# Kernel tuning notes

Hardware: AMD Instinct MI355X
Metric: run time of the kernel (lower is better)

## Reference

```python
import jax, jax.numpy as jnp
import numpy as np

EPS = 1e-5
GROUPS = 32


def conv1x1(x, W, b):
    # x: (B,C,T), W: (O,C), b: (O,)
    return jnp.einsum('bct,oc->bot', x, W) + b[None, :, None]


def group_norm(x, gamma, beta):
    B, C, T = x.shape
    xg = x.reshape(B, GROUPS, (C // GROUPS) * T)
    mu = xg.mean(axis=-1, keepdims=True)
    var = xg.var(axis=-1, keepdims=True)
    xn = ((xg - mu) * jax.lax.rsqrt(var + EPS)).reshape(B, C, T)
    return xn * gamma[None, :, None] + beta[None, :, None]


def block(x, W, b, gamma, beta):
    return jax.nn.relu(group_norm(conv1x1(x, W, b), gamma, beta))


def setup_inputs() -> dict:
    key = jax.random.key(0)
    ks = jax.random.split(key, 8)
    B, C, P, T, TF = 4, 512, 512, 2048, 4096
    inp = {
        'feature': jax.random.normal(ks[0], (B, C, T), jnp.float32),
        'frame_level_feature': jax.random.uniform(ks[1], (B, C, TF), jnp.float32),
        # cur_point_conv: conv1x1 C->P + GN(32,P)
        'W1': jax.random.normal(ks[2], (P, C), jnp.float32) / np.sqrt(C),
        'b1': jnp.zeros((P,), jnp.float32),
        'g1': jnp.ones((P,), jnp.float32),
        'be1': jnp.zeros((P,), jnp.float32),
        # lr_conv: conv1x1 C->2P + GN(32,2P)
        'W2': jax.random.normal(ks[3], (2 * P, C), jnp.float32) / np.sqrt(C),
        'b2': jnp.zeros((2 * P,), jnp.float32),
        'g2': jnp.ones((2 * P,), jnp.float32),
        'be2': jnp.zeros((2 * P,), jnp.float32),
        # proposal_conv: conv1x1 4P->C + GN(32,C)
        'W3': jax.random.normal(ks[4], (C, 4 * P), jnp.float32) / np.sqrt(4 * P),
        'b3': jnp.zeros((C,), jnp.float32),
        'g3': jnp.ones((C,), jnp.float32),
        'be3': jnp.zeros((C,), jnp.float32),
    }
    return inp


def reference(feature, frame_level_feature, W1, b1, g1, be1, W2, b2, g2, be2, W3, b3, g3, be3):
    fm_short = block(feature, W1, b1, g1, be1)          # (B,P,T)
    feat = block(feature, W2, b2, g2, be2)              # (B,2P,T)
    t = feature.shape[2]
    # inverse-CDF resampling (uses batch 0 statistics, as original)
    mean_values = frame_level_feature.mean(axis=1)[0]   # (TF,)
    mean_values = mean_values / mean_values.sum()
    cdf = (jnp.cumsum(mean_values) * t).astype(jnp.int32)
    cdf = jnp.minimum(cdf, t - 1)                       # (TF,)
    # exact vectorization of findNearNum loop: first index with minimal |cdf-i|
    targets = jnp.arange(t, dtype=jnp.int32)
    idx = jnp.argmin(jnp.abs(cdf[None, :] - targets[:, None]), axis=1)  # (t,)
    sampled = frame_level_feature[:, :, idx]            # (B,C,t)
    mixed = jnp.concatenate([sampled, feat, fm_short], axis=1)  # (B,4P,t)
    mixed = block(mixed, W3, b3, g3, be3)               # (B,C,t)
    return (mixed, feat)
```

## Files before the change

kernel.cpp:

```cpp
#include <hip/hip_runtime.h>

typedef unsigned short u16;
typedef unsigned int   u32;
typedef __attribute__((ext_vector_type(8))) short short8;
typedef __attribute__((ext_vector_type(4))) float f32x4;

__device__ __forceinline__ float bf2f(u16 v) {
  return __uint_as_float(((u32)v) << 16);
}
__device__ __forceinline__ u16 f2bf(float f) {
  u32 u = __float_as_uint(f);
  u32 r = (u + 0x7FFFu + ((u >> 16) & 1u)) >> 16;
  return (u16)r;
}
__device__ __forceinline__ float relu(float x) { return x < 0.f ? 0.f : x; }

__device__ __forceinline__ void gld16(const void* g, void* l) {
  __builtin_amdgcn_global_load_lds((const __attribute__((address_space(1))) u32*)g,
                                   (__attribute__((address_space(3))) u32*)l, 16, 0, 0);
}

__global__ void colmean_part_kernel(const float* __restrict__ frame,
                                    double* __restrict__ partD) {
  int tf = blockIdx.x * 256 + threadIdx.x;
  int ch = blockIdx.y;
  const float* f0 = frame + tf + (size_t)ch * 64 * 4096;
  double s = 0.0;
  for (int c = 0; c < 64; ++c) s += (double)f0[(size_t)c * 4096];
  partD[ch * 4096 + tf] = s;
}

__global__ void scanD_kernel(const double* __restrict__ partD, int* __restrict__ cdf) {
  __shared__ double part[256];
  __shared__ double base[256];
  __shared__ double Ss;
  int tid = threadIdx.x;
  double loc[16];
  double s = 0.0;
#pragma unroll
  for (int i = 0; i < 16; ++i) {
    int tf = tid * 16 + i;
    double m = 0.0;
#pragma unroll
    for (int ch = 0; ch < 8; ++ch) m += partD[ch * 4096 + tf];
    loc[i] = m / 512.0;
    s += loc[i];
  }
  part[tid] = s;
  __syncthreads();
  if (tid == 0) {
    double t = 0.0;
    for (int i = 0; i < 256; ++i) t += part[i];
    Ss = t;
  }
  __syncthreads();
  double S = Ss;
  s = 0.0;
#pragma unroll
  for (int i = 0; i < 16; ++i) { loc[i] = loc[i] / S; s += loc[i]; }
  part[tid] = s;
  __syncthreads();
  if (tid == 0) {
    double c = 0.0;
    for (int i = 0; i < 256; ++i) { base[i] = c; c += part[i]; }
  }
  __syncthreads();
  double c = base[tid];
#pragma unroll
  for (int i = 0; i < 16; ++i) {
    c += loc[i];
    int iv = (int)(c * 2048.0);
    cdf[tid * 16 + i] = iv < 2047 ? iv : 2047;
  }
}

__global__ void argmin_kernel(const int* __restrict__ cdf, int* __restrict__ idx) {
  __shared__ int sd[256], sj[256];
  int target = blockIdx.x;
  int tid = threadIdx.x;
  int best = 0x7fffffff, bj = 0x7fffffff;
  for (int j = tid; j < 4096; j += 256) {
    int d = cdf[j] - target; d = d < 0 ? -d : d;
    if (d < best) { best = d; bj = j; }
  }
  sd[tid] = best; sj[tid] = bj;
  __syncthreads();
  for (int s = 128; s > 0; s >>= 1) {
    if (tid < s) {
      if (sd[tid+s] < sd[tid] || (sd[tid+s] == sd[tid] && sj[tid+s] < sj[tid])) {
        sd[tid] = sd[tid+s]; sj[tid] = sj[tid+s];
      }
    }
    __syncthreads();
  }
  if (tid == 0) idx[target] = sj[0];
}

__global__ void gatherT_kernel(const float* __restrict__ frame, const int* __restrict__ idx,
                               u16* __restrict__ X3T) {
  __shared__ u16 tile[64][65];
  __shared__ int sidx[64];
  int cb = blockIdx.x * 64, t0 = blockIdx.y * 64, b = blockIdx.z;
  int tid = threadIdx.x;
  if (tid < 64) {
    int it = idx[t0 + tid];
    sidx[tid] = it < 0 ? 0 : (it > 4095 ? 4095 : it);
  }
  __syncthreads();
  const float* fb = frame + (size_t)b * 512 * 4096;
  for (int i = tid; i < 4096; i += 256) {
    int r = i >> 6, tt = i & 63;
    tile[tt][r] = f2bf(fb[(size_t)(cb + r) * 4096 + sidx[tt]]);
  }
  __syncthreads();
  u16* xb = X3T + (size_t)b * 2048 * 2048;
  for (int i = tid; i < 4096; i += 256) {
    int r = i >> 6, cc = i & 63;
    xb[(size_t)(t0 + r) * 2048 + cb + cc] = tile[r][cc];
  }
}

__global__ void transposeCT_kernel(const float* __restrict__ X, u16* __restrict__ XT) {
  __shared__ u16 tile[64][65];
  int cb = blockIdx.x * 64, t0 = blockIdx.y * 64, b = blockIdx.z;
  int tid = threadIdx.x;
  const float* xb = X + (size_t)b * 512 * 2048;
  for (int i = tid; i < 4096; i += 256) {
    int r = i >> 6, tt = i & 63;
    tile[tt][r] = f2bf(xb[(size_t)(cb + r) * 2048 + t0 + tt]);
  }
  __syncthreads();
  u16* xtb = XT + (size_t)b * 2048 * 512;
  for (int i = tid; i < 4096; i += 256) {
    int r = i >> 6, cc = i & 63;
    xtb[(size_t)(t0 + r) * 512 + cb + cc] = tile[r][cc];
  }
}

__global__ void convW12_kernel(const float* __restrict__ W1, const float* __restrict__ W2,
                               u16* __restrict__ dst) {
  int i = blockIdx.x * 256 + threadIdx.x;
  dst[i] = f2bf(i < 262144 ? W1[i] : W2[i - 262144]);
}
__global__ void convW_kernel(const float* __restrict__ src, u16* __restrict__ dst, int n) {
  int i = blockIdx.x * 256 + threadIdx.x;
  if (i < n) dst[i] = f2bf(src[i]);
}

__global__ __launch_bounds__(128) void gemm12_kernel(
    const u16* __restrict__ A, const u16* __restrict__ Bt,
    const float* __restrict__ b1, const float* __restrict__ b2,
    float* __restrict__ Y, float* __restrict__ raw1, float* __restrict__ raw2)
{
  const int K = 512;
  __shared__ short As[2][2048];
  __shared__ short Bs[2][4096];
  const int tid = threadIdx.x;
  const int lane = tid & 63;
  const int w = tid >> 6;
  const int nt = blockIdx.x, mt = blockIdx.y, bb = blockIdx.z;
  const u16* Ab = A + (size_t)mt * 64 * K;
  const u16* Bb = Bt + ((size_t)bb * 2048 + (size_t)nt * 128) * K;
  const int lm = lane & 15, lq = lane >> 4;
  f32x4 acc[4][4] = {};

  auto stage = [&](int buf, int kt) {
#pragma unroll
    for (int p = 0; p < 2; ++p) {
      int chunk = tid + 128 * p;
      int row = chunk >> 2;
      int ko = ((chunk & 3) ^ ((row >> 1) & 3)) << 3;
      gld16(Ab + (size_t)row * K + kt + ko, (char*)As[buf] + chunk * 16);
    }
#pragma unroll
    for (int p = 0; p < 4; ++p) {
      int chunk = tid + 128 * p;
      int row = chunk >> 2;
      int ko = ((chunk & 3) ^ ((row >> 1) & 3)) << 3;
      gld16(Bb + (size_t)row * K + kt + ko, (char*)Bs[buf] + chunk * 16);
    }
  };

  stage(0, 0);
  for (int s = 0; s < 16; ++s) {
    int cur = s & 1;
    __syncthreads();
    if (s + 1 < 16) stage(cur ^ 1, (s + 1) << 5);
    short8 af[4], bfv[4];
#pragma unroll
    for (int i = 0; i < 4; ++i) {
      int r = i * 16 + lm;
      af[i] = *(const short8*)(As[cur] + r * 32 + ((lq ^ ((r >> 1) & 3)) << 3));
    }
#pragma unroll
    for (int j = 0; j < 4; ++j) {
      int r = w * 64 + j * 16 + lm;
      bfv[j] = *(const short8*)(Bs[cur] + r * 32 + ((lq ^ ((r >> 1) & 3)) << 3));
    }
#pragma unroll
    for (int i = 0; i < 4; ++i)
#pragma unroll
      for (int j = 0; j < 4; ++j)
        acc[i][j] = __builtin_amdgcn_mfma_f32_16x16x32_bf16(af[i], bfv[j], acc[i][j], 0, 0, 0);
  }

  float s1[4] = {0.f, 0.f, 0.f, 0.f};
  float s2[4] = {0.f, 0.f, 0.f, 0.f};
#pragma unroll
  for (int i = 0; i < 4; ++i) {
    int mbase = mt * 64 + i * 16 + lq * 4;
#pragma unroll
    for (int e = 0; e < 4; ++e) {
      int m = mbase + e;
      float bv = m < 512 ? b1[m] : b2[m - 512];
      float* yp = Y + ((size_t)bb * 1536 + m) * 2048 + nt * 128 + w * 64 + lm;
#pragma unroll
      for (int j = 0; j < 4; ++j) {
        float v = acc[i][j][e] + bv;
        yp[j * 16] = v;
        s1[i] += v; s2[i] += v * v;
      }
    }
  }
#pragma unroll
  for (int i = 0; i < 4; ++i) {
#pragma unroll
    for (int off = 32; off > 0; off >>= 1) {
      s1[i] += __shfl_xor(s1[i], off);
      s2[i] += __shfl_xor(s2[i], off);
    }
  }
  if (lane == 0) {
    if (mt < 8) {
#pragma unroll
      for (int i = 0; i < 4; ++i) {
        int g = mt * 4 + i;
        atomicAdd(&raw1[(bb * 32 + g) * 2],     s1[i]);
        atomicAdd(&raw1[(bb * 32 + g) * 2 + 1], s2[i]);
      }
    } else {
#pragma unroll
      for (int i = 0; i < 2; ++i) {
        int g = (mt - 8) * 2 + i;
        atomicAdd(&raw2[(bb * 32 + g) * 2],     s1[2 * i] + s1[2 * i + 1]);
        atomicAdd(&raw2[(bb * 32 + g) * 2 + 1], s2[2 * i] + s2[2 * i + 1]);
      }
    }
  }
}

__global__ __launch_bounds__(128) void gemm3s_kernel(
    const u16* __restrict__ A, const u16* __restrict__ Bt,
    const float* __restrict__ bias, float* __restrict__ Yp)
{
  const int K = 2048;
  __shared__ short As[2][2048];
  __shared__ short Bs[2][4096];
  const int tid = threadIdx.x;
  const int lane = tid & 63;
  const int w = tid >> 6;
  const int nt = blockIdx.x, mt = blockIdx.y;
  const int bb = blockIdx.z >> 1, ks = blockIdx.z & 1;
  const u16* Ab = A + (size_t)mt * 64 * K + ks * 1024;
  const u16* Bb = Bt + ((size_t)bb * 2048 + (size_t)nt * 128) * K + ks * 1024;
  const int lm = lane & 15, lq = lane >> 4;
  f32x4 acc[4][4] = {};

  auto stage = [&](int buf, int kt) {
#pragma unroll
    for (int p = 0; p < 2; ++p) {
      int chunk = tid + 128 * p;
      int row = chunk >> 2;
      int ko = ((chunk & 3) ^ ((row >> 1) & 3)) << 3;
      gld16(Ab + (size_t)row * K + kt + ko, (char*)As[buf] + chunk * 16);
    }
#pragma unroll
    for (int p = 0; p < 4; ++p) {
      int chunk = tid + 128 * p;
      int row = chunk >> 2;
      int ko = ((chunk & 3) ^ ((row >> 1) & 3)) << 3;
      gld16(Bb + (size_t)row * K + kt + ko, (char*)Bs[buf] + chunk * 16);
    }
  };

  stage(0, 0);
  for (int s = 0; s < 32; ++s) {
    int cur = s & 1;
    __syncthreads();
    if (s + 1 < 32) stage(cur ^ 1, (s + 1) << 5);
    short8 af[4], bfv[4];
#pragma unroll
    for (int i = 0; i < 4; ++i) {
      int r = i * 16 + lm;
      af[i] = *(const short8*)(As[cur] + r * 32 + ((lq ^ ((r >> 1) & 3)) << 3));
    }
#pragma unroll
    for (int j = 0; j < 4; ++j) {
      int r = w * 64 + j * 16 + lm;
      bfv[j] = *(const short8*)(Bs[cur] + r * 32 + ((lq ^ ((r >> 1) & 3)) << 3));
    }
#pragma unroll
    for (int i = 0; i < 4; ++i)
#pragma unroll
      for (int j = 0; j < 4; ++j)
        acc[i][j] = __builtin_amdgcn_mfma_f32_16x16x32_bf16(af[i], bfv[j], acc[i][j], 0, 0, 0);
  }
#pragma unroll
  for (int i = 0; i < 4; ++i) {
    int mbase = mt * 64 + i * 16 + lq * 4;
#pragma unroll
    for (int e = 0; e < 4; ++e) {
      int m = mbase + e;
      float bv = ks ? 0.f : bias[m];
      float* yp = Yp + ((size_t)(ks * 4 + bb) * 512 + m) * 2048 + nt * 128 + w * 64 + lm;
#pragma unroll
      for (int j = 0; j < 4; ++j)
        yp[j * 16] = acc[i][j][e] + bv;
    }
  }
}

__global__ void stats3p_kernel(const float* __restrict__ Yp, float* __restrict__ raw) {
  int chunk = blockIdx.x, g = blockIdx.y, b = blockIdx.z, tid = threadIdx.x;
  const float* base = Yp + ((size_t)b * 512 + g * 16) * 2048 + (size_t)chunk * 4096;
  float s = 0.f, ss = 0.f;
#pragma unroll
  for (int i = 0; i < 16; ++i) {
    int o = tid + 256 * i;
    float v = base[o] + base[o + 4194304];
    s += v; ss += v * v;
  }
  __shared__ float s1[256], s2[256];
  s1[tid] = s; s2[tid] = ss;
  __syncthreads();
  for (int st = 128; st > 0; st >>= 1) {
    if (tid < st) { s1[tid] += s1[tid + st]; s2[tid] += s2[tid + st]; }
    __syncthreads();
  }
  if (tid == 0) {
    atomicAdd(&raw[(b * 32 + g) * 2],     s1[0]);
    atomicAdd(&raw[(b * 32 + g) * 2 + 1], s2[0]);
  }
}

__global__ void statsFin12_kernel(const float* __restrict__ raw1, const float* __restrict__ raw2,
                                  float* __restrict__ st1, float* __restrict__ st2) {
  int i = threadIdx.x;
  const float* raw = i < 128 ? raw1 : raw2;
  float* st = i < 128 ? st1 : st2;
  int j = i & 127;
  float n = i < 128 ? 32768.f : 65536.f;
  float mu = raw[j * 2] / n;
  float var = raw[j * 2 + 1] / n - mu * mu;
  st[j * 2] = mu;
  st[j * 2 + 1] = 1.0f / sqrtf(var + 1e-5f);
}
__global__ void statsFin_kernel(const float* __restrict__ raw, float* __restrict__ stats,
                                float n) {
  int i = threadIdx.x;
  float mu = raw[i * 2] / n;
  float var = raw[i * 2 + 1] / n - mu * mu;
  stats[i * 2] = mu;
  stats[i * 2 + 1] = 1.0f / sqrtf(var + 1e-5f);
}

__global__ void normT_kernel(const float* __restrict__ Y, const float* __restrict__ stats,
                             const float* __restrict__ gamma, const float* __restrict__ beta,
                             int rowsB, int chBase, int C, int gShift,
                             u16* __restrict__ X3T, int colBase,
                             float* __restrict__ featOut) {
  __shared__ u16 tile[64][65];
  int b = blockIdx.z, c0 = blockIdx.y * 64, t0 = blockIdx.x * 64;
  const float* yb = Y + ((size_t)b * rowsB + chBase) * 2048;
  for (int i = threadIdx.x; i < 4096; i += 256) {
    int r = i >> 6, cc = i & 63;
    int ch = c0 + r;
    int gI = (b * 32 + (ch >> gShift)) * 2;
    float mu = stats[gI], rs = stats[gI + 1];
    float v = yb[(size_t)ch * 2048 + t0 + cc];
    float o = relu((v - mu) * rs * gamma[ch] + beta[ch]);
    tile[cc][r] = f2bf(o);
    if (featOut) featOut[((size_t)b * C + ch) * 2048 + t0 + cc] = o;
  }
  __syncthreads();
  for (int i = threadIdx.x; i < 4096; i += 256) {
    int r = i >> 6, cc = i & 63;
    X3T[((size_t)b * 2048 + t0 + r) * 2048 + colBase + c0 + cc] = tile[r][cc];
  }
}

__global__ void norm3_kernel(const float* __restrict__ Yp, const float* __restrict__ stats,
                             const float* __restrict__ gamma, const float* __restrict__ beta,
                             float* __restrict__ out) {
  int i = blockIdx.x * 256 + threadIdx.x;
  int b = i >> 20;
  int ch = (i >> 11) & 511;
  int gI = (b * 32 + (ch >> 4)) * 2;
  float mu = stats[gI], rs = stats[gI + 1];
  float v = Yp[i] + Yp[i + 4194304];
  out[i] = relu((v - mu) * rs * gamma[ch] + beta[ch]);
}

extern "C" void kernel_launch(void* const* d_in, const int* in_sizes, int n_in,
                              void* d_out, int out_size, void* d_ws, size_t ws_size,
                              hipStream_t stream) {
  const float* feature = (const float*)d_in[0];
  const float* frame   = (const float*)d_in[1];
  const float* W1 = (const float*)d_in[2];
  const float* b1 = (const float*)d_in[3];
  const float* g1 = (const float*)d_in[4];
  const float* be1 = (const float*)d_in[5];
  const float* W2 = (const float*)d_in[6];
  const float* b2 = (const float*)d_in[7];
  const float* g2 = (const float*)d_in[8];
  const float* be2 = (const float*)d_in[9];
  const float* W3 = (const float*)d_in[10];
  const float* b3 = (const float*)d_in[11];
  const float* g3 = (const float*)d_in[12];
  const float* be3 = (const float*)d_in[13];

  char* ws = (char*)d_ws;
  u16*    X3T   = (u16*)(ws + 0);
  float*  Y12f  = (float*)(ws + 33554432);
  float*  Y3p   = (float*)(ws + 33554432);
  u16*    W3b   = (u16*)(ws + 67108864);
  double* partD = (double*)(ws + 50331648);
  u16*    featT = (u16*)(ws + 83886080);
  u16*    W12b  = (u16*)(ws + 92274688);
  int*    cdf   = (int*)(ws + 93847552);
  int*    idx   = (int*)(ws + 93863936);
  float*  raw1  = (float*)(ws + 93872128);
  float*  raw2  = (float*)(ws + 93873152);
  float*  raw3  = (float*)(ws + 93874176);
  float*  st1   = (float*)(ws + 93875200);
  float*  st2   = (float*)(ws + 93876224);
  float*  st3   = (float*)(ws + 93877248);

  float* outMixed = (float*)d_out;
  float* outFeat  = outMixed + (size_t)4 * 512 * 2048;

  hipMemsetAsync(raw1, 0, 3 * 1024, stream);

  colmean_part_kernel<<<dim3(16, 8), 256, 0, stream>>>(frame, partD);
  scanD_kernel<<<1, 256, 0, stream>>>(partD, cdf);
  argmin_kernel<<<2048, 256, 0, stream>>>(cdf, idx);
  gatherT_kernel<<<dim3(8, 32, 4), 256, 0, stream>>>(frame, idx, X3T);
  transposeCT_kernel<<<dim3(8, 32, 4), 256, 0, stream>>>(feature, featT);

  convW12_kernel<<<3072, 256, 0, stream>>>(W1, W2, W12b);
  gemm12_kernel<<<dim3(16, 24, 4), 128, 0, stream>>>(W12b, featT, b1, b2, Y12f,
                                                     raw1, raw2);
  statsFin12_kernel<<<1, 256, 0, stream>>>(raw1, raw2, st1, st2);
  normT_kernel<<<dim3(32, 8, 4), 256, 0, stream>>>(Y12f, st1, g1, be1, 1536, 0, 512, 4,
                                                   X3T, 1536, (float*)nullptr);
  normT_kernel<<<dim3(32, 16, 4), 256, 0, stream>>>(Y12f, st2, g2, be2, 1536, 512, 1024, 5,
                                                    X3T, 512, outFeat);
  convW_kernel<<<4096, 256, 0, stream>>>(W3, W3b, 1048576);
  gemm3s_kernel<<<dim3(16, 8, 8), 128, 0, stream>>>(W3b, X3T, b3, Y3p);
  stats3p_kernel<<<dim3(8, 32, 4), 256, 0, stream>>>(Y3p, raw3);
  statsFin_kernel<<<1, 128, 0, stream>>>(raw3, st3, 32768.f);
  norm3_kernel<<<16384, 256, 0, stream>>>(Y3p, st3, g3, be3, outMixed);
}
```

Before: 283.3 us.

## Fuse final GEMM with group-norm stats and normalize via grid barrier

The third GEMM drops split-K and its partial-output buffer. Each block now reduces group-norm sums from its accumulators, adds them atomically, waits at a global spin barrier over all 512 blocks, then writes the normalized ReLU output directly. The stats, stats-finalize and norm passes and their round trips to memory are removed, and the K tile doubles to 64. The statsFin kernels for the first two GEMMs are also folded into normT. The grid barrier assumes every block is co-resident (512 blocks of 128 threads with 48KB LDS), which risks deadlock, and halving the grid reduces parallelism.

```diff
diff --git a/kernel.cpp b/kernel.cpp
--- a/kernel.cpp
+++ b/kernel.cpp
@@ -249,37 +249,40 @@
   }
 }
 
-__global__ __launch_bounds__(128) void gemm3s_kernel(
+__global__ __launch_bounds__(128) void gemm3f_kernel(
     const u16* __restrict__ A, const u16* __restrict__ Bt,
-    const float* __restrict__ bias, float* __restrict__ Yp)
+    const float* __restrict__ bias,
+    const float* __restrict__ g3, const float* __restrict__ be3,
+    float* __restrict__ raw3, int* __restrict__ bar,
+    float* __restrict__ out)
 {
   const int K = 2048;
-  __shared__ short As[2][2048];
-  __shared__ short Bs[2][4096];
+  __shared__ char smem[49152];
+  short* As0 = (short*)smem;
+  short* Bs0 = (short*)(smem + 16384);
   const int tid = threadIdx.x;
   const int lane = tid & 63;
   const int w = tid >> 6;
-  const int nt = blockIdx.x, mt = blockIdx.y;
-  const int bb = blockIdx.z >> 1, ks = blockIdx.z & 1;
-  const u16* Ab = A + (size_t)mt * 64 * K + ks * 1024;
-  const u16* Bb = Bt + ((size_t)bb * 2048 + (size_t)nt * 128) * K + ks * 1024;
+  const int nt = blockIdx.x, mt = blockIdx.y, bb = blockIdx.z;
+  const u16* Ab = A + (size_t)mt * 64 * K;
+  const u16* Bb = Bt + ((size_t)bb * 2048 + (size_t)nt * 128) * K;
   const int lm = lane & 15, lq = lane >> 4;
   f32x4 acc[4][4] = {};
 
   auto stage = [&](int buf, int kt) {
 #pragma unroll
-    for (int p = 0; p < 2; ++p) {
-      int chunk = tid + 128 * p;
-      int row = chunk >> 2;
-      int ko = ((chunk & 3) ^ ((row >> 1) & 3)) << 3;
-      gld16(Ab + (size_t)row * K + kt + ko, (char*)As[buf] + chunk * 16);
-    }
-#pragma unroll
     for (int p = 0; p < 4; ++p) {
       int chunk = tid + 128 * p;
-      int row = chunk >> 2;
-      int ko = ((chunk & 3) ^ ((row >> 1) & 3)) << 3;
-      gld16(Bb + (size_t)row * K + kt + ko, (char*)Bs[buf] + chunk * 16);
+      int row = chunk >> 3, seg = chunk & 7;
+      gld16(Ab + (size_t)row * K + kt + ((seg ^ (row & 7)) << 3),
+            (char*)(As0 + buf * 4096) + chunk * 16);
+    }
+#pragma unroll
+    for (int p = 0; p < 8; ++p) {
+      int chunk = tid + 128 * p;
+      int row = chunk >> 3, seg = chunk & 7;
+      gld16(Bb + (size_t)row * K + kt + ((seg ^ (row & 7)) << 3),
+            (char*)(Bs0 + buf * 8192) + chunk * 16);
     }
   };
 
@@ -287,84 +290,96 @@
   for (int s = 0; s < 32; ++s) {
     int cur = s & 1;
     __syncthreads();
-    if (s + 1 < 32) stage(cur ^ 1, (s + 1) << 5);
-    short8 af[4], bfv[4];
-#pragma unroll
-    for (int i = 0; i < 4; ++i) {
-      int r = i * 16 + lm;
-      af[i] = *(const short8*)(As[cur] + r * 32 + ((lq ^ ((r >> 1) & 3)) << 3));
-    }
-#pragma unroll
-    for (int j = 0; j < 4; ++j) {
-      int r = w * 64 + j * 16 + lm;
-      bfv[j] = *(const short8*)(Bs[cur] + r * 32 + ((lq ^ ((r >> 1) & 3)) << 3));
-    }
-#pragma unroll
-    for (int i = 0; i < 4; ++i)
-#pragma unroll
-      for (int j = 0; j < 4; ++j)
-        acc[i][j] = __builtin_amdgcn_mfma_f32_16x16x32_bf16(af[i], bfv[j], acc[i][j], 0, 0, 0);
-  }
+    if (s + 1 < 32) stage(cur ^ 1, (s + 1) << 6);
+    const short* Asc = As0 + cur * 4096;
+    const short* Bsc = Bs0 + cur * 8192;
+#pragma unroll
+    for (int kk = 0; kk < 2; ++kk) {
+      short8 af[4], bfv[4];
+#pragma unroll
+      for (int i = 0; i < 4; ++i) {
+        int r = i * 16 + lm;
+        af[i] = *(const short8*)(Asc + r * 64 + (((kk * 4 + lq) ^ (r & 7)) << 3));
+      }
+#pragma unroll
+      for (int j = 0; j < 4; ++j) {
+        int r = w * 64 + j * 16 + lm;
+        bfv[j] = *(const short8*)(Bsc + r * 64 + (((kk * 4 + lq) ^ (r & 7)) << 3));
+      }
+#pragma unroll
+      for (int i = 0; i < 4; ++i)
+#pragma unroll
+        for (int j = 0; j < 4; ++j)
+          acc[i][j] = __builtin_amdgcn_mfma_f32_16x16x32_bf16(af[i], bfv[j], acc[i][j], 0, 0, 0);
+    }
+  }
+
+  float s1[4] = {0.f, 0.f, 0.f, 0.f};
+  float s2[4] = {0.f, 0.f, 0.f, 0.f};
 #pragma unroll
   for (int i = 0; i < 4; ++i) {
     int mbase = mt * 64 + i * 16 + lq * 4;
 #pragma unroll
     for (int e = 0; e < 4; ++e) {
-      int m = mbase + e;
-      float bv = ks ? 0.f : bias[m];
-      float* yp = Yp + ((size_t)(ks * 4 + bb) * 512 + m) * 2048 + nt * 128 + w * 64 + lm;
+      float bv = bias[mbase + e];
+#pragma unroll
+      for (int j = 0; j < 4; ++j) {
+        acc[i][j][e] += bv;
+        float v = acc[i][j][e];
+        s1[i] += v; s2[i] += v * v;
+      }
+    }
+  }
+#pragma unroll
+  for (int i = 0; i < 4; ++i) {
+#pragma unroll
+    for (int off = 32; off > 0; off >>= 1) {
+      s1[i] += __shfl_xor(s1[i], off);
+      s2[i] += __shfl_xor(s2[i], off);
+    }
+  }
+  if (lane == 0) {
+#pragma unroll
+    for (int i = 0; i < 4; ++i) {
+      int g = mt * 4 + i;
+      atomicAdd(&raw3[(bb * 32 + g) * 2],     s1[i]);
+      atomicAdd(&raw3[(bb * 32 + g) * 2 + 1], s2[i]);
+    }
+    __threadfence();
+  }
+
+  __syncthreads();
+  if (tid == 0) {
+    __hip_atomic_fetch_add(bar, 1, __ATOMIC_RELEASE, __HIP_MEMORY_SCOPE_AGENT);
+    while (__hip_atomic_load(bar, __ATOMIC_ACQUIRE, __HIP_MEMORY_SCOPE_AGENT) < 512) {
+      __builtin_amdgcn_s_sleep(8);
+    }
+  }
+  __syncthreads();
+
+#pragma unroll
+  for (int i = 0; i < 4; ++i) {
+    int g = mt * 4 + i;
+    float sA = __hip_atomic_load(&raw3[(bb * 32 + g) * 2],     __ATOMIC_RELAXED,
+                                 __HIP_MEMORY_SCOPE_AGENT);
+    float sB = __hip_atomic_load(&raw3[(bb * 32 + g) * 2 + 1], __ATOMIC_RELAXED,
+                                 __HIP_MEMORY_SCOPE_AGENT);
+    float mu = sA * (1.f / 32768.f);
+    float rs = 1.0f / sqrtf(sB * (1.f / 32768.f) - mu * mu + 1e-5f);
+#pragma unroll
+    for (int e = 0; e < 4; ++e) {
+      int m = mt * 64 + i * 16 + lq * 4 + e;
+      float ga = g3[m], bt = be3[m];
+      float* yp = out + ((size_t)bb * 512 + m) * 2048 + nt * 128 + w * 64 + lm;
 #pragma unroll
       for (int j = 0; j < 4; ++j)
-        yp[j * 16] = acc[i][j][e] + bv;
-    }
-  }
-}
-
-__global__ void stats3p_kernel(const float* __restrict__ Yp, float* __restrict__ raw) {
-  int chunk = blockIdx.x, g = blockIdx.y, b = blockIdx.z, tid = threadIdx.x;
-  const float* base = Yp + ((size_t)b * 512 + g * 16) * 2048 + (size_t)chunk * 4096;
-  float s = 0.f, ss = 0.f;
-#pragma unroll
-  for (int i = 0; i < 16; ++i) {
-    int o = tid + 256 * i;
-    float v = base[o] + base[o + 4194304];
-    s += v; ss += v * v;
-  }
-  __shared__ float s1[256], s2[256];
-  s1[tid] = s; s2[tid] = ss;
-  __syncthreads();
-  for (int st = 128; st > 0; st >>= 1) {
-    if (tid < st) { s1[tid] += s1[tid + st]; s2[tid] += s2[tid + st]; }
-    __syncthreads();
-  }
-  if (tid == 0) {
-    atomicAdd(&raw[(b * 32 + g) * 2],     s1[0]);
-    atomicAdd(&raw[(b * 32 + g) * 2 + 1], s2[0]);
-  }
-}
-
-__global__ void statsFin12_kernel(const float* __restrict__ raw1, const float* __restrict__ raw2,
-                                  float* __restrict__ st1, float* __restrict__ st2) {
-  int i = threadIdx.x;
-  const float* raw = i < 128 ? raw1 : raw2;
-  float* st = i < 128 ? st1 : st2;
-  int j = i & 127;
-  float n = i < 128 ? 32768.f : 65536.f;
-  float mu = raw[j * 2] / n;
-  float var = raw[j * 2 + 1] / n - mu * mu;
-  st[j * 2] = mu;
-  st[j * 2 + 1] = 1.0f / sqrtf(var + 1e-5f);
-}
-__global__ void statsFin_kernel(const float* __restrict__ raw, float* __restrict__ stats,
-                                float n) {
-  int i = threadIdx.x;
-  float mu = raw[i * 2] / n;
-  float var = raw[i * 2 + 1] / n - mu * mu;
-  stats[i * 2] = mu;
-  stats[i * 2 + 1] = 1.0f / sqrtf(var + 1e-5f);
-}
-
-__global__ void normT_kernel(const float* __restrict__ Y, const float* __restrict__ stats,
+        yp[j * 16] = relu((acc[i][j][e] - mu) * rs * ga + bt);
+    }
+  }
+}
+
+__global__ void normT_kernel(const float* __restrict__ Y, const float* __restrict__ raw,
+                             float inv_n,
                              const float* __restrict__ gamma, const float* __restrict__ beta,
                              int rowsB, int chBase, int C, int gShift,
                              u16* __restrict__ X3T, int colBase,
@@ -376,7 +391,9 @@
     int r = i >> 6, cc = i & 63;
     int ch = c0 + r;
     int gI = (b * 32 + (ch >> gShift)) * 2;
-    float mu = stats[gI], rs = stats[gI + 1];
+    float mu = raw[gI] * inv_n;
+    float var = raw[gI + 1] * inv_n - mu * mu;
+    float rs = 1.0f / sqrtf(var + 1e-5f);
     float v = yb[(size_t)ch * 2048 + t0 + cc];
     float o = relu((v - mu) * rs * gamma[ch] + beta[ch]);
     tile[cc][r] = f2bf(o);
@@ -387,18 +404,6 @@
     int r = i >> 6, cc = i & 63;
     X3T[((size_t)b * 2048 + t0 + r) * 2048 + colBase + c0 + cc] = tile[r][cc];
   }
-}
-
-__global__ void norm3_kernel(const float* __restrict__ Yp, const float* __restrict__ stats,
-                             const float* __restrict__ gamma, const float* __restrict__ beta,
-                             float* __restrict__ out) {
-  int i = blockIdx.x * 256 + threadIdx.x;
-  int b = i >> 20;
-  int ch = (i >> 11) & 511;
-  int gI = (b * 32 + (ch >> 4)) * 2;
-  float mu = stats[gI], rs = stats[gI + 1];
-  float v = Yp[i] + Yp[i + 4194304];
-  out[i] = relu((v - mu) * rs * gamma[ch] + beta[ch]);
 }
 
 extern "C" void kernel_launch(void* const* d_in, const int* in_sizes, int n_in,
@@ -422,7 +427,6 @@
   char* ws = (char*)d_ws;
   u16*    X3T   = (u16*)(ws + 0);
   float*  Y12f  = (float*)(ws + 33554432);
-  float*  Y3p   = (float*)(ws + 33554432);
   u16*    W3b   = (u16*)(ws + 67108864);
   double* partD = (double*)(ws + 50331648);
   u16*    featT = (u16*)(ws + 83886080);
@@ -432,14 +436,12 @@
   float*  raw1  = (float*)(ws + 93872128);
   float*  raw2  = (float*)(ws + 93873152);
   float*  raw3  = (float*)(ws + 93874176);
-  float*  st1   = (float*)(ws + 93875200);
-  float*  st2   = (float*)(ws + 93876224);
-  float*  st3   = (float*)(ws + 93877248);
+  int*    bar   = (int*)(ws + 93875200);
 
   float* outMixed = (float*)d_out;
   float* outFeat  = outMixed + (size_t)4 * 512 * 2048;
 
-  hipMemsetAsync(raw1, 0, 3 * 1024, stream);
+  hipMemsetAsync(raw1, 0, 4 * 1024, stream);
 
   colmean_part_kernel<<<dim3(16, 8), 256, 0, stream>>>(frame, partD);
   scanD_kernel<<<1, 256, 0, stream>>>(partD, cdf);
@@ -450,14 +452,13 @@
   convW12_kernel<<<3072, 256, 0, stream>>>(W1, W2, W12b);
   gemm12_kernel<<<dim3(16, 24, 4), 128, 0, stream>>>(W12b, featT, b1, b2, Y12f,
                                                      raw1, raw2);
-  statsFin12_kernel<<<1, 256, 0, stream>>>(raw1, raw2, st1, st2);
-  normT_kernel<<<dim3(32, 8, 4), 256, 0, stream>>>(Y12f, st1, g1, be1, 1536, 0, 512, 4,
+  normT_kernel<<<dim3(32, 8, 4), 256, 0, stream>>>(Y12f, raw1, 1.f / 32768.f,
+                                                   g1, be1, 1536, 0, 512, 4,
                                                    X3T, 1536, (float*)nullptr);
-  normT_kernel<<<dim3(32, 16, 4), 256, 0, stream>>>(Y12f, st2, g2, be2, 1536, 512, 1024, 5,
+  normT_kernel<<<dim3(32, 16, 4), 256, 0, stream>>>(Y12f, raw2, 1.f / 65536.f,
+                                                    g2, be2, 1536, 512, 1024, 5,
                                                     X3T, 512, outFeat);
   convW_kernel<<<4096, 256, 0, stream>>>(W3, W3b, 1048576);
-  gemm3s_kernel<<<dim3(16, 8, 8), 128, 0, stream>>>(W3b, X3T, b3, Y3p);
-  stats3p_kernel<<<dim3(8, 32, 4), 256, 0, stream>>>(Y3p, raw3);
-  statsFin_kernel<<<1, 128, 0, stream>>>(raw3, st3, 32768.f);
-  norm3_kernel<<<16384, 256, 0, stream>>>(Y3p, st3, g3, be3, outMixed);
-}
+  gemm3f_kernel<<<dim3(16, 8, 4), 128, 0, stream>>>(W3b, X3T, b3, g3, be3,
+                                                    raw3, bar, outMixed);
+}
```

Measured after the change: 362.7 us. +28.0%, slower.
